# Kernel optimization log

Hardware: AMD Instinct MI355X
Metric: run time of the kernel (lower is better)

The kernel has to match this reference:

```python
import jax, jax.numpy as jnp
import numpy as np

N_NODES = 20000
N_EDGES = 640000
IN_NODE = 128
IN_EDGE = 16
HIDDEN = 64
OUT = 128
HEADS = 4
N_GRAPHS = 64
NEG_SLOPE = 0.2


def _glorot(key, shape):
    fan_in, fan_out = shape[0], shape[-1]
    s = jnp.sqrt(6.0 / (fan_in + fan_out)).astype(jnp.float32)
    return jax.random.uniform(key, shape, jnp.float32, -s, s)


def setup_inputs() -> dict:
    key = jax.random.key(0)
    ks = jax.random.split(key, 32)
    inp = {
        "x": jax.random.normal(ks[0], (N_NODES, IN_NODE), jnp.float32),
        "edge_attr": jax.random.normal(ks[1], (N_EDGES, IN_EDGE), jnp.float32),
        "edge_index": jax.random.randint(ks[2], (2, N_EDGES), 0, N_NODES),
        "batch": jnp.sort(jax.random.randint(ks[3], (N_NODES,), 0, N_GRAPHS)),
    }
    # layer dims: (in, out_per_head, concat)
    dims = [(IN_NODE, HIDDEN, True), (HIDDEN * HEADS, HIDDEN, True), (HIDDEN * HEADS, OUT, False)]
    k = 4
    for i, (cin, cout, concat) in enumerate(dims):
        hc = HEADS * cout
        inp[f"Wl{i}"] = _glorot(ks[k], (cin, hc)); k += 1
        inp[f"bl{i}"] = jnp.zeros((hc,), jnp.float32)
        inp[f"Wr{i}"] = _glorot(ks[k], (cin, hc)); k += 1
        inp[f"br{i}"] = jnp.zeros((hc,), jnp.float32)
        inp[f"We{i}"] = _glorot(ks[k], (IN_EDGE, hc)); k += 1
        inp[f"att{i}"] = _glorot(ks[k], (HEADS, cout)); k += 1
        inp[f"bias{i}"] = jnp.zeros((hc if concat else cout,), jnp.float32)
    return inp


def _gatv2_layer(x, edge_index, edge_attr, Wl, bl, Wr, br, We, att, bias, concat):
    """One PyG-style GATv2Conv layer with edge features."""
    H, C = att.shape
    N = x.shape[0]
    src, dst = edge_index[0], edge_index[1]
    xl = (x @ Wl + bl).reshape(N, H, C)  # messages from source
    xr = (x @ Wr + br).reshape(N, H, C)  # target query
    e = (edge_attr @ We).reshape(-1, H, C)
    m = jax.nn.leaky_relu(xl[src] + xr[dst] + e, NEG_SLOPE)  # [E,H,C]
    logits = jnp.einsum("ehc,hc->eh", m, att)  # [E,H]
    # scatter-softmax over edges grouped by destination node
    lmax = jax.ops.segment_max(logits, dst, num_segments=N)
    p = jnp.exp(logits - lmax[dst])
    denom = jax.ops.segment_sum(p, dst, num_segments=N)
    alpha = p / (denom[dst] + 1e-16)  # [E,H]
    out = jax.ops.segment_sum(alpha[:, :, None] * xl[src], dst, num_segments=N)  # [N,H,C]
    if concat:
        return out.reshape(N, H * C) + bias
    return out.mean(axis=1) + bias


def reference(x, edge_attr, edge_index, batch,
              Wl0, bl0, Wr0, br0, We0, att0, bias0,
              Wl1, bl1, Wr1, br1, We1, att1, bias1,
              Wl2, bl2, Wr2, br2, We2, att2, bias2):
    layers = [
        (Wl0, bl0, Wr0, br0, We0, att0, bias0, True),
        (Wl1, bl1, Wr1, br1, We1, att1, bias1, True),
        (Wl2, bl2, Wr2, br2, We2, att2, bias2, False),
    ]
    h = x
    for (Wl, bl, Wr, br, We, att, b, concat) in layers:
        h = _gatv2_layer(h, edge_index, edge_attr, Wl, bl, Wr, br, We, att, b, concat)
    # global max + mean pooling per graph
    x_max = jax.ops.segment_max(h, batch, num_segments=N_GRAPHS)
    s = jax.ops.segment_sum(h, batch, num_segments=N_GRAPHS)
    cnt = jax.ops.segment_sum(jnp.ones((h.shape[0], 1), h.dtype), batch, num_segments=N_GRAPHS)
    x_mean = s / jnp.maximum(cnt, 1.0)
    return jnp.concatenate([x_max, x_mean], axis=1)  # [G, 2*OUT]
```

## Files before the change

### kernel.cpp

```cpp
#include <hip/hip_runtime.h>

#define NB 8

typedef float f32x2 __attribute__((ext_vector_type(2)));

template <int K, int M>
__global__ __launch_bounds__(256) void node_gemm(
    const float* __restrict__ X, const float* __restrict__ W,
    const float* __restrict__ bias, float* __restrict__ Y) {
  constexpr int NPB = 16;
  constexpr int COLS4 = M / 4;
  constexpr int NG = 256 / COLS4;
  constexpr int RPN = NPB / NG;
  __shared__ float xs[NPB * K];
  const int tid = threadIdx.x;
  const int n0 = blockIdx.x * NPB;
  {
    const float4* X4 = reinterpret_cast<const float4*>(X + (size_t)n0 * K);
    float4* xs4 = reinterpret_cast<float4*>(xs);
    for (int i = tid; i < NPB * K / 4; i += 256) xs4[i] = X4[i];
  }
  __syncthreads();
  const int c4 = (tid % COLS4) * 4;
  const int r0 = (tid / COLS4) * RPN;
  float acc[RPN][4];
#pragma unroll
  for (int r = 0; r < RPN; ++r)
#pragma unroll
    for (int q = 0; q < 4; ++q) acc[r][q] = 0.f;

  for (int k = 0; k < K; k += 4) {
    float xv[RPN][4];
#pragma unroll
    for (int r = 0; r < RPN; ++r)
      *reinterpret_cast<float4*>(xv[r]) =
          *reinterpret_cast<const float4*>(&xs[(r0 + r) * K + k]);
#pragma unroll
    for (int j = 0; j < 4; ++j) {
      float wv[4];
      *reinterpret_cast<float4*>(wv) =
          *reinterpret_cast<const float4*>(&W[(size_t)(k + j) * M + c4]);
#pragma unroll
      for (int r = 0; r < RPN; ++r)
#pragma unroll
        for (int q = 0; q < 4; ++q)
          acc[r][q] = fmaf(xv[r][j], wv[q], acc[r][q]);
    }
  }
  float bv[4];
  *reinterpret_cast<float4*>(bv) = *reinterpret_cast<const float4*>(&bias[c4]);
#pragma unroll
  for (int r = 0; r < RPN; ++r) {
    float o[4];
#pragma unroll
    for (int q = 0; q < 4; ++q) o[q] = acc[r][q] + bv[q];
    *reinterpret_cast<float4*>(&Y[(size_t)(n0 + r0 + r) * M + c4]) =
        *reinterpret_cast<float4*>(o);
  }
}

__global__ void hist_b(const int* __restrict__ ei, int* __restrict__ kcnt,
                       int E, int bdiv) {
  int i = blockIdx.x * blockDim.x + threadIdx.x;
  if (i < E) atomicAdd(&kcnt[ei[E + i] * NB + ei[i] / bdiv], 1);
}

__global__ __launch_bounds__(1024) void blk_scan(
    const int* __restrict__ in, int* __restrict__ out1, int* __restrict__ bsum, int n) {
  __shared__ int buf[1024];
  const int tid = threadIdx.x;
  const int gid = blockIdx.x * 1024 + tid;
  int v = (gid < n) ? in[gid] : 0;
  buf[tid] = v;
  __syncthreads();
  for (int off = 1; off < 1024; off <<= 1) {
    int t = (tid >= off) ? buf[tid - off] : 0;
    __syncthreads();
    buf[tid] += t;
    __syncthreads();
  }
  if (gid < n) out1[gid] = buf[tid];
  if (tid == 1023) bsum[blockIdx.x] = buf[1023];
}

__global__ __launch_bounds__(256) void scan_bsum(int* __restrict__ bsum, int nb) {
  __shared__ int buf[256];
  const int tid = threadIdx.x;
  int v = (tid < nb) ? bsum[tid] : 0;
  buf[tid] = v;
  __syncthreads();
  for (int off = 1; off < 256; off <<= 1) {
    int t = (tid >= off) ? buf[tid - off] : 0;
    __syncthreads();
    buf[tid] += t;
    __syncthreads();
  }
  if (tid < nb) bsum[tid] = buf[tid];
}

__global__ void add_off(int* __restrict__ kptr, const int* __restrict__ bsum, int n) {
  int gid = blockIdx.x * blockDim.x + threadIdx.x;
  if (gid == 0) kptr[0] = 0;
  if (gid < n) {
    int blk = gid >> 10;
    if (blk > 0) kptr[1 + gid] += bsum[blk - 1];
  }
}

__global__ void csr_fill_b(const int* __restrict__ ei, const int* __restrict__ kptr,
                           int* __restrict__ kfill, int* __restrict__ csr_src,
                           int* __restrict__ csr_eid, int E, int bdiv) {
  int i = blockIdx.x * blockDim.x + threadIdx.x;
  if (i < E) {
    int src = ei[i], dst = ei[E + i];
    int key = dst * NB + src / bdiv;
    int slot = kptr[key] + atomicAdd(&kfill[key], 1);
    csr_src[slot] = src;
    csr_eid[slot] = i;
  }
}

__global__ void ea_perm(const float* __restrict__ ea, const int* __restrict__ csr_eid,
                        float* __restrict__ ea_csr, int E) {
  int i = blockIdx.x * blockDim.x + threadIdx.x;
  if (i < E * 16) {
    int slot = i >> 4;
    ea_csr[i] = ea[((size_t)csr_eid[slot] << 4) + (i & 15)];
  }
}

__global__ void graph_bounds(const int* __restrict__ batch, int* __restrict__ gstart,
                             int* __restrict__ gend, int N) {
  int i = blockIdx.x * blockDim.x + threadIdx.x;
  if (i < N) {
    int g = batch[i];
    atomicMin(&gstart[g], i);
    atomicMax(&gend[g], i + 1);
  }
}

template <int GS>
__device__ __forceinline__ void gat_edge_pk(
    const float4 a, const double (&c)[8], const float4 xrv,
    const f32x2 (&w01)[16], const f32x2 (&w23)[16], const float (&attv)[4],
    float& m, float& s, float (&acc)[4]) {
  f32x2 m01, m23;
  m01.x = a.x + xrv.x; m01.y = a.y + xrv.y;
  m23.x = a.z + xrv.z; m23.y = a.w + xrv.w;
#pragma unroll
  for (int i = 0; i < 8; ++i) {
    asm("v_pk_fma_f32 %0, %2, %3, %0 op_sel:[0,0,0] op_sel_hi:[0,1,1]\n\t"
        "v_pk_fma_f32 %1, %2, %4, %1 op_sel:[0,0,0] op_sel_hi:[0,1,1]\n\t"
        "v_pk_fma_f32 %0, %2, %5, %0 op_sel:[1,0,0] op_sel_hi:[1,1,1]\n\t"
        "v_pk_fma_f32 %1, %2, %6, %1 op_sel:[1,0,0] op_sel_hi:[1,1,1]"
        : "+v"(m01), "+v"(m23)
        : "s"(c[i]), "v"(w01[2 * i]), "v"(w23[2 * i]),
          "v"(w01[2 * i + 1]), "v"(w23[2 * i + 1]));
  }
  const float mv[4] = {m01.x, m01.y, m23.x, m23.y};
  float l = 0.f;
#pragma unroll
  for (int q = 0; q < 4; ++q) {
    const float v = fmaxf(mv[q], 0.2f * mv[q]);
    l = fmaf(v, attv[q], l);
  }
#pragma unroll
  for (int off = 1; off < GS; off <<= 1) l += __shfl_xor(l, off);
  const float nm = fmaxf(m, l);
  const float sc = __expf(m - nm);
  const float pe = __expf(l - nm);
  m = nm;
  s = fmaf(s, sc, pe);
  acc[0] = fmaf(pe, a.x, acc[0] * sc);
  acc[1] = fmaf(pe, a.y, acc[1] * sc);
  acc[2] = fmaf(pe, a.z, acc[2] * sc);
  acc[3] = fmaf(pe, a.w, acc[3] * sc);
}

template <int HCROW, int MODE>
__global__ __launch_bounds__(256) void fused_gat(
    const float* __restrict__ xl, const float* __restrict__ xr,
    const float* __restrict__ ea_csr, const float* __restrict__ We,
    const float* __restrict__ att, const float* __restrict__ bias,
    const int* __restrict__ kptr, const int* __restrict__ csr_src,
    float* __restrict__ out, float* __restrict__ outB, int N) {
  constexpr int C = HCROW / 4;
  constexpr int GS = C / 4;
  const int lane = threadIdx.x & 63;
  const int wslot = threadIdx.x >> 6;
  int bx = blockIdx.x;
  int colbase = 0;
  float* o_ptr = out;
  if (MODE == 1) {
    const int gb = gridDim.x >> 1;
    if (bx >= gb) { bx -= gb; colbase = 256; o_ptr = outB; }
  }
  const int dst = bx * 4 + wslot;
  if (dst >= N) return;

  f32x2 w01[16], w23[16];
#pragma unroll
  for (int k = 0; k < 16; ++k) {
    const float4 t =
        *reinterpret_cast<const float4*>(&We[k * HCROW + colbase + lane * 4]);
    w01[k].x = t.x; w01[k].y = t.y;
    w23[k].x = t.z; w23[k].y = t.w;
  }
  const int col0 = colbase + lane * 4;
  const int head = col0 / C;
  float attv[4];
  *reinterpret_cast<float4*>(attv) =
      *reinterpret_cast<const float4*>(&att[head * C + (col0 % C)]);
  const float4* xl4 = reinterpret_cast<const float4*>(xl);
  const int rs4 = HCROW / 4;
  const int coff = col0 >> 2;
  const float4 xrv =
      reinterpret_cast<const float4*>(xr)[(size_t)dst * rs4 + coff];
  const double* ed = reinterpret_cast<const double*>(ea_csr);

  const int row0 = __builtin_amdgcn_readfirstlane(kptr[dst * NB]);
  const int rend = __builtin_amdgcn_readfirstlane(kptr[dst * NB + NB]);

  float m = -__builtin_inff(), s = 0.f;
  float acc[4] = {0.f, 0.f, 0.f, 0.f};

  if (row0 < rend) {
    const int last = rend - 1;
    const int s0 = csr_src[row0];
    const int s1 = csr_src[min(row0 + 1, last)];
    const int s2 = csr_src[min(row0 + 2, last)];
    const int s3 = csr_src[min(row0 + 3, last)];
    float4 a0 = xl4[(size_t)s0 * rs4 + coff];
    float4 a1 = xl4[(size_t)s1 * rs4 + coff];
    float4 a2 = xl4[(size_t)s2 * rs4 + coff];
    float4 a3 = xl4[(size_t)s3 * rs4 + coff];
    int sr0 = csr_src[min(row0 + 4, last)];
    int sr1 = csr_src[min(row0 + 5, last)];
    double c0[8], c1[8];
    {
      const double* e0 = ed + (size_t)row0 * 8;
      const double* e1 = ed + (size_t)min(row0 + 1, last) * 8;
#pragma unroll
      for (int k = 0; k < 8; ++k) { c0[k] = e0[k]; c1[k] = e1[k]; }
    }

    for (int p = row0; p < rend; p += 2) {
      const float4 na0 = xl4[(size_t)sr0 * rs4 + coff];
      const float4 na1 = xl4[(size_t)sr1 * rs4 + coff];
      const int nsr0 = csr_src[min(p + 6, last)];
      const int nsr1 = csr_src[min(p + 7, last)];
      double cn0[8], cn1[8];
      {
        const double* e0 = ed + (size_t)min(p + 2, last) * 8;
        const double* e1 = ed + (size_t)min(p + 3, last) * 8;
#pragma unroll
        for (int k = 0; k < 8; ++k) { cn0[k] = e0[k]; cn1[k] = e1[k]; }
      }
      gat_edge_pk<GS>(a0, c0, xrv, w01, w23, attv, m, s, acc);
      if (p + 1 < rend) gat_edge_pk<GS>(a1, c1, xrv, w01, w23, attv, m, s, acc);
      a0 = a2; a1 = a3; a2 = na0; a3 = na1;
      sr0 = nsr0; sr1 = nsr1;
#pragma unroll
      for (int k = 0; k < 8; ++k) { c0[k] = cn0[k]; c1[k] = cn1[k]; }
    }
  }

  const float inv = 1.f / (s + 1e-16f);
  float o[4];
  if (MODE == 0) {
    float bv[4];
    *reinterpret_cast<float4*>(bv) = *reinterpret_cast<const float4*>(&bias[col0]);
#pragma unroll
    for (int q = 0; q < 4; ++q) o[q] = fmaf(acc[q], inv, bv[q]);
    *reinterpret_cast<float4*>(&o_ptr[(size_t)dst * HCROW + col0]) =
        *reinterpret_cast<float4*>(o);
  } else {
#pragma unroll
    for (int q = 0; q < 4; ++q) {
      o[q] = acc[q] * inv;
      o[q] += __shfl_xor(o[q], 32);
    }
    if (lane < 32)
      *reinterpret_cast<float4*>(&o_ptr[(size_t)dst * 128 + lane * 4]) =
          *reinterpret_cast<float4*>(o);
  }
}

__global__ __launch_bounds__(256) void pool_graph(
    const float* __restrict__ hA, const float* __restrict__ hB,
    const float* __restrict__ bias2, const int* __restrict__ gstart,
    const int* __restrict__ gend, float* __restrict__ out) {
  const int g = blockIdx.x;
  const int c = threadIdx.x & 127;
  const int sub = threadIdx.x >> 7;
  const int s0 = gstart[g], e0 = gend[g];
  const float b = bias2[c];
  float mx = -__builtin_inff(), sm = 0.f;
  for (int n = s0 + sub; n < e0; n += 2) {
    const float v = fmaf(0.25f, hA[(size_t)n * 128 + c] + hB[(size_t)n * 128 + c], b);
    mx = fmaxf(mx, v);
    sm += v;
  }
  __shared__ float smx[128], ssm[128];
  if (sub) { smx[c] = mx; ssm[c] = sm; }
  __syncthreads();
  if (!sub) {
    mx = fmaxf(mx, smx[c]);
    sm += ssm[c];
    const int cnt = e0 - s0;
    out[g * 256 + c] = (cnt > 0) ? mx : 0.f;
    out[g * 256 + 128 + c] = sm / fmaxf((float)cnt, 1.f);
  }
}

extern "C" void kernel_launch(void* const* d_in, const int* in_sizes, int n_in,
                              void* d_out, int out_size, void* d_ws, size_t ws_size,
                              hipStream_t stream) {
  const float* x     = (const float*)d_in[0];
  const float* ea    = (const float*)d_in[1];
  const int*   ei    = (const int*)d_in[2];
  const int*   batch = (const int*)d_in[3];
  const int N = in_sizes[0] / 128;
  const int E = in_sizes[2] / 2;
  const int NBINS = N * NB;
  const int bdiv = (N + NB - 1) / NB;

  const float* Wl[3]   = {(const float*)d_in[4],  (const float*)d_in[11], (const float*)d_in[18]};
  const float* blv[3]  = {(const float*)d_in[5],  (const float*)d_in[12], (const float*)d_in[19]};
  const float* Wr[3]   = {(const float*)d_in[6],  (const float*)d_in[13], (const float*)d_in[20]};
  const float* brv[3]  = {(const float*)d_in[7],  (const float*)d_in[14], (const float*)d_in[21]};
  const float* Wev[3]  = {(const float*)d_in[8],  (const float*)d_in[15], (const float*)d_in[22]};
  const float* attv[3] = {(const float*)d_in[9],  (const float*)d_in[16], (const float*)d_in[23]};
  const float* bias[3] = {(const float*)d_in[10], (const float*)d_in[17], (const float*)d_in[24]};

  float* ws = (float*)d_ws;
  float* xl     = ws;
  float* xr     = xl + (size_t)N * 512;
  float* ea_csr = xr + (size_t)N * 512;
  float* h      = ea_csr + (size_t)E * 16;
  int* kptr     = (int*)(h + (size_t)N * 256);
  int* csr_src  = kptr + (NBINS + 1);
  int* bsum     = csr_src + E;
  int* gstart   = bsum + 257;
  int* gend     = gstart + 64;
  int* csr_eid = (int*)h;
  int* kcnt    = csr_eid + E;
  int* kfill   = kcnt + NBINS;
  float* hsumA = h;
  float* hsumB = h + (size_t)N * 128;
  (void)n_in; (void)out_size; (void)ws_size;

  const int nodeBlocks = N / 16;
  const int edgeBlocks = (E + 255) / 256;
  const int scanBlocks = (NBINS + 1023) / 1024;
  const int gatBlocks = (N + 3) / 4;

  hipMemsetAsync(kcnt, 0, (size_t)2 * NBINS * sizeof(int), stream);
  hipMemsetAsync(gstart, 0x7f, 64 * sizeof(int), stream);
  hipMemsetAsync(gend, 0, 64 * sizeof(int), stream);
  hist_b<<<edgeBlocks, 256, 0, stream>>>(ei, kcnt, E, bdiv);
  graph_bounds<<<(N + 255) / 256, 256, 0, stream>>>(batch, gstart, gend, N);
  blk_scan<<<scanBlocks, 1024, 0, stream>>>(kcnt, kptr + 1, bsum, NBINS);
  scan_bsum<<<1, 256, 0, stream>>>(bsum, scanBlocks);
  add_off<<<(NBINS + 255) / 256, 256, 0, stream>>>(kptr, bsum, NBINS);
  csr_fill_b<<<edgeBlocks, 256, 0, stream>>>(ei, kptr, kfill, csr_src, csr_eid, E, bdiv);
  ea_perm<<<(E * 16 + 255) / 256, 256, 0, stream>>>(ea, csr_eid, ea_csr, E);

  node_gemm<128, 256><<<nodeBlocks, 256, 0, stream>>>(x, Wl[0], blv[0], xl);
  node_gemm<128, 256><<<nodeBlocks, 256, 0, stream>>>(x, Wr[0], brv[0], xr);
  fused_gat<256, 0><<<gatBlocks, 256, 0, stream>>>(
      xl, xr, ea_csr, Wev[0], attv[0], bias[0], kptr, csr_src, h, nullptr, N);

  node_gemm<256, 256><<<nodeBlocks, 256, 0, stream>>>(h, Wl[1], blv[1], xl);
  node_gemm<256, 256><<<nodeBlocks, 256, 0, stream>>>(h, Wr[1], brv[1], xr);
  fused_gat<256, 0><<<gatBlocks, 256, 0, stream>>>(
      xl, xr, ea_csr, Wev[1], attv[1], bias[1], kptr, csr_src, h, nullptr, N);

  node_gemm<256, 512><<<nodeBlocks, 256, 0, stream>>>(h, Wl[2], blv[2], xl);
  node_gemm<256, 512><<<nodeBlocks, 256, 0, stream>>>(h, Wr[2], brv[2], xr);
  fused_gat<512, 1><<<2 * gatBlocks, 256, 0, stream>>>(
      xl, xr, ea_csr, Wev[2], attv[2], bias[2], kptr, csr_src, hsumA, hsumB, N);

  pool_graph<<<64, 256, 0, stream>>>(hsumA, hsumB, bias[2], gstart, gend, (float*)d_out);
}
```

Baseline: 1.112 ms.

## Stage edge attributes in LDS chunks with double buffering in fused GAT

Edge attributes are no longer read by every lane as uniform scalar double loads. Each wave now cooperatively loads chunks of 32 edges' attributes into shared memory, prefetching the next chunk into registers while the current one is processed. The packed FMA takes its edge coefficient from a VGPR instead of an SGPR, and mode-1 blocks are interleaved so both column halves of a node run on adjacent blocks. NB is doubled (finer key binning) and the block-sum scan is widened to match. The cost is LDS traffic and VGPR pressure in exchange for fewer scalar memory loads.

```diff
diff --git a/kernel.cpp b/kernel.cpp
--- a/kernel.cpp
+++ b/kernel.cpp
@@ -1,6 +1,7 @@
 #include <hip/hip_runtime.h>
 
-#define NB 8
+#define NB 16
+#define CHUNK 32
 
 typedef float f32x2 __attribute__((ext_vector_type(2)));
 
@@ -83,13 +84,13 @@
   if (tid == 1023) bsum[blockIdx.x] = buf[1023];
 }
 
-__global__ __launch_bounds__(256) void scan_bsum(int* __restrict__ bsum, int nb) {
-  __shared__ int buf[256];
+__global__ __launch_bounds__(1024) void scan_bsum(int* __restrict__ bsum, int nb) {
+  __shared__ int buf[1024];
   const int tid = threadIdx.x;
   int v = (tid < nb) ? bsum[tid] : 0;
   buf[tid] = v;
   __syncthreads();
-  for (int off = 1; off < 256; off <<= 1) {
+  for (int off = 1; off < 1024; off <<= 1) {
     int t = (tid >= off) ? buf[tid - off] : 0;
     __syncthreads();
     buf[tid] += t;
@@ -141,7 +142,7 @@
 
 template <int GS>
 __device__ __forceinline__ void gat_edge_pk(
-    const float4 a, const double (&c)[8], const float4 xrv,
+    const float4 a, const f32x2 (&c)[8], const float4 xrv,
     const f32x2 (&w01)[16], const f32x2 (&w23)[16], const float (&attv)[4],
     float& m, float& s, float (&acc)[4]) {
   f32x2 m01, m23;
@@ -154,7 +155,7 @@
         "v_pk_fma_f32 %0, %2, %5, %0 op_sel:[1,0,0] op_sel_hi:[1,1,1]\n\t"
         "v_pk_fma_f32 %1, %2, %6, %1 op_sel:[1,0,0] op_sel_hi:[1,1,1]"
         : "+v"(m01), "+v"(m23)
-        : "s"(c[i]), "v"(w01[2 * i]), "v"(w23[2 * i]),
+        : "v"(c[i]), "v"(w01[2 * i]), "v"(w23[2 * i]),
           "v"(w01[2 * i + 1]), "v"(w23[2 * i + 1]));
   }
   const float mv[4] = {m01.x, m01.y, m23.x, m23.y};
@@ -186,14 +187,16 @@
     float* __restrict__ out, float* __restrict__ outB, int N) {
   constexpr int C = HCROW / 4;
   constexpr int GS = C / 4;
+  __shared__ float ea_s[4][2][CHUNK * 16];
   const int lane = threadIdx.x & 63;
   const int wslot = threadIdx.x >> 6;
   int bx = blockIdx.x;
   int colbase = 0;
   float* o_ptr = out;
   if (MODE == 1) {
-    const int gb = gridDim.x >> 1;
-    if (bx >= gb) { bx -= gb; colbase = 256; o_ptr = outB; }
+    colbase = (bx & 1) * 256;
+    if (bx & 1) o_ptr = outB;
+    bx >>= 1;
   }
   const int dst = bx * 4 + wslot;
   if (dst >= N) return;
@@ -216,7 +219,6 @@
   const int coff = col0 >> 2;
   const float4 xrv =
       reinterpret_cast<const float4*>(xr)[(size_t)dst * rs4 + coff];
-  const double* ed = reinterpret_cast<const double*>(ea_csr);
 
   const int row0 = __builtin_amdgcn_readfirstlane(kptr[dst * NB]);
   const int rend = __builtin_amdgcn_readfirstlane(kptr[dst * NB + NB]);
@@ -226,42 +228,57 @@
 
   if (row0 < rend) {
     const int last = rend - 1;
-    const int s0 = csr_src[row0];
-    const int s1 = csr_src[min(row0 + 1, last)];
-    const int s2 = csr_src[min(row0 + 2, last)];
-    const int s3 = csr_src[min(row0 + 3, last)];
-    float4 a0 = xl4[(size_t)s0 * rs4 + coff];
-    float4 a1 = xl4[(size_t)s1 * rs4 + coff];
-    float4 a2 = xl4[(size_t)s2 * rs4 + coff];
-    float4 a3 = xl4[(size_t)s3 * rs4 + coff];
-    int sr0 = csr_src[min(row0 + 4, last)];
-    int sr1 = csr_src[min(row0 + 5, last)];
-    double c0[8], c1[8];
     {
-      const double* e0 = ed + (size_t)row0 * 8;
-      const double* e1 = ed + (size_t)min(row0 + 1, last) * 8;
-#pragma unroll
-      for (int k = 0; k < 8; ++k) { c0[k] = e0[k]; c1[k] = e1[k]; }
+      const int n4 = min(CHUNK, rend - row0) * 4;
+      const float4* esrc = reinterpret_cast<const float4*>(ea_csr + (size_t)row0 * 16);
+      float4* ed = reinterpret_cast<float4*>(ea_s[wslot][0]);
+      if (lane < n4) ed[lane] = esrc[lane];
+      if (lane + 64 < n4) ed[lane + 64] = esrc[lane + 64];
     }
-
-    for (int p = row0; p < rend; p += 2) {
-      const float4 na0 = xl4[(size_t)sr0 * rs4 + coff];
-      const float4 na1 = xl4[(size_t)sr1 * rs4 + coff];
-      const int nsr0 = csr_src[min(p + 6, last)];
-      const int nsr1 = csr_src[min(p + 7, last)];
-      double cn0[8], cn1[8];
-      {
-        const double* e0 = ed + (size_t)min(p + 2, last) * 8;
-        const double* e1 = ed + (size_t)min(p + 3, last) * 8;
-#pragma unroll
-        for (int k = 0; k < 8; ++k) { cn0[k] = e0[k]; cn1[k] = e1[k]; }
+    int buf = 0;
+    for (int cs = row0; cs < rend; cs += CHUNK) {
+      const int cn = min(CHUNK, rend - cs);
+      float4 t0, t1;
+      int nn4 = 0;
+      if (cs + CHUNK < rend) {
+        nn4 = min(CHUNK, rend - (cs + CHUNK)) * 4;
+        const float4* esrc =
+            reinterpret_cast<const float4*>(ea_csr + (size_t)(cs + CHUNK) * 16);
+        if (lane < nn4) t0 = esrc[lane];
+        if (lane + 64 < nn4) t1 = esrc[lane + 64];
       }
-      gat_edge_pk<GS>(a0, c0, xrv, w01, w23, attv, m, s, acc);
-      if (p + 1 < rend) gat_edge_pk<GS>(a1, c1, xrv, w01, w23, attv, m, s, acc);
-      a0 = a2; a1 = a3; a2 = na0; a3 = na1;
-      sr0 = nsr0; sr1 = nsr1;
-#pragma unroll
-      for (int k = 0; k < 8; ++k) { c0[k] = cn0[k]; c1[k] = cn1[k]; }
+      const f32x2* eb = reinterpret_cast<const f32x2*>(ea_s[wslot][buf]);
+
+      int s0 = csr_src[cs];
+      int s1 = csr_src[min(cs + 1, last)];
+      float4 a0 = xl4[(size_t)s0 * rs4 + coff];
+      float4 a1 = xl4[(size_t)s1 * rs4 + coff];
+      int sr0 = csr_src[min(cs + 2, last)];
+      int sr1 = csr_src[min(cs + 3, last)];
+
+      for (int j = 0; j < cn; j += 2) {
+        const float4 na0 = xl4[(size_t)sr0 * rs4 + coff];
+        const float4 na1 = xl4[(size_t)sr1 * rs4 + coff];
+        const int nsr0 = csr_src[min(cs + j + 4, last)];
+        const int nsr1 = csr_src[min(cs + j + 5, last)];
+        f32x2 c0[8], c1[8];
+#pragma unroll
+        for (int i = 0; i < 8; ++i) {
+          c0[i] = eb[j * 8 + i];
+          c1[i] = eb[(j + 1) * 8 + i];
+        }
+        gat_edge_pk<GS>(a0, c0, xrv, w01, w23, attv, m, s, acc);
+        if (j + 1 < cn) gat_edge_pk<GS>(a1, c1, xrv, w01, w23, attv, m, s, acc);
+        a0 = na0; a1 = na1;
+        sr0 = nsr0; sr1 = nsr1;
+      }
+
+      if (nn4 > 0) {
+        float4* ed = reinterpret_cast<float4*>(ea_s[wslot][buf ^ 1]);
+        if (lane < nn4) ed[lane] = t0;
+        if (lane + 64 < nn4) ed[lane + 64] = t1;
+        buf ^= 1;
+      }
     }
   }
 
@@ -341,7 +358,7 @@
   int* kptr     = (int*)(h + (size_t)N * 256);
   int* csr_src  = kptr + (NBINS + 1);
   int* bsum     = csr_src + E;
-  int* gstart   = bsum + 257;
+  int* gstart   = bsum + 1024;
   int* gend     = gstart + 64;
   int* csr_eid = (int*)h;
   int* kcnt    = csr_eid + E;
@@ -361,7 +378,7 @@
   hist_b<<<edgeBlocks, 256, 0, stream>>>(ei, kcnt, E, bdiv);
   graph_bounds<<<(N + 255) / 256, 256, 0, stream>>>(batch, gstart, gend, N);
   blk_scan<<<scanBlocks, 1024, 0, stream>>>(kcnt, kptr + 1, bsum, NBINS);
-  scan_bsum<<<1, 256, 0, stream>>>(bsum, scanBlocks);
+  scan_bsum<<<1, 1024, 0, stream>>>(bsum, scanBlocks);
   add_off<<<(NBINS + 255) / 256, 256, 0, stream>>>(kptr, bsum, NBINS);
   csr_fill_b<<<edgeBlocks, 256, 0, stream>>>(ei, kptr, kfill, csr_src, csr_eid, E, bdiv);
   ea_perm<<<(E * 16 + 255) / 256, 256, 0, stream>>>(ea, csr_eid, ea_csr, E);
```

After: 1.152 ms. 3.6% more time.

## Split each destination's edge list across two waves with online-softmax merge

Applied to the files above, without the earlier changes.

Each destination node is now processed by two waves, each covering half of its CSR edge range, and their partial softmax states (max, sum, accumulators) are merged through shared memory. This doubles wave-level parallelism and halves per-wave serial edge latency in the fused GAT kernel. The CSR bin factor NB also goes from 8 to 16, and the bsum scan buffer and workspace offset are enlarged to match. The cost is an extra block sync, shared-memory traffic, and twice the per-wave setup, including the We register loads.

```diff
diff --git a/kernel.cpp b/kernel.cpp
--- a/kernel.cpp
+++ b/kernel.cpp
@@ -1,6 +1,6 @@
 #include <hip/hip_runtime.h>
 
-#define NB 8
+#define NB 16
 
 typedef float f32x2 __attribute__((ext_vector_type(2)));
 
@@ -83,13 +83,13 @@
   if (tid == 1023) bsum[blockIdx.x] = buf[1023];
 }
 
-__global__ __launch_bounds__(256) void scan_bsum(int* __restrict__ bsum, int nb) {
-  __shared__ int buf[256];
+__global__ __launch_bounds__(1024) void scan_bsum(int* __restrict__ bsum, int nb) {
+  __shared__ int buf[1024];
   const int tid = threadIdx.x;
   int v = (tid < nb) ? bsum[tid] : 0;
   buf[tid] = v;
   __syncthreads();
-  for (int off = 1; off < 256; off <<= 1) {
+  for (int off = 1; off < 1024; off <<= 1) {
     int t = (tid >= off) ? buf[tid - off] : 0;
     __syncthreads();
     buf[tid] += t;
@@ -186,17 +186,20 @@
     float* __restrict__ out, float* __restrict__ outB, int N) {
   constexpr int C = HCROW / 4;
   constexpr int GS = C / 4;
+  __shared__ float mrg[2][64][6];
   const int lane = threadIdx.x & 63;
   const int wslot = threadIdx.x >> 6;
+  const int dpair = wslot >> 1;
+  const int half = wslot & 1;
   int bx = blockIdx.x;
   int colbase = 0;
   float* o_ptr = out;
   if (MODE == 1) {
-    const int gb = gridDim.x >> 1;
-    if (bx >= gb) { bx -= gb; colbase = 256; o_ptr = outB; }
-  }
-  const int dst = bx * 4 + wslot;
-  if (dst >= N) return;
+    colbase = (bx & 1) * 256;
+    if (bx & 1) o_ptr = outB;
+    bx >>= 1;
+  }
+  const int dst = bx * 2 + dpair;
 
   f32x2 w01[16], w23[16];
 #pragma unroll
@@ -218,8 +221,11 @@
       reinterpret_cast<const float4*>(xr)[(size_t)dst * rs4 + coff];
   const double* ed = reinterpret_cast<const double*>(ea_csr);
 
-  const int row0 = __builtin_amdgcn_readfirstlane(kptr[dst * NB]);
-  const int rend = __builtin_amdgcn_readfirstlane(kptr[dst * NB + NB]);
+  const int r0f = __builtin_amdgcn_readfirstlane(kptr[dst * NB]);
+  const int rendf = __builtin_amdgcn_readfirstlane(kptr[dst * NB + NB]);
+  const int mid = r0f + ((rendf - r0f + 1) >> 1);
+  const int row0 = half ? mid : r0f;
+  const int rend = half ? rendf : mid;
 
   float m = -__builtin_inff(), s = 0.f;
   float acc[4] = {0.f, 0.f, 0.f, 0.f};
@@ -265,6 +271,28 @@
     }
   }
 
+  if (half) {
+    mrg[dpair][lane][0] = m;
+    mrg[dpair][lane][1] = s;
+    mrg[dpair][lane][2] = acc[0];
+    mrg[dpair][lane][3] = acc[1];
+    mrg[dpair][lane][4] = acc[2];
+    mrg[dpair][lane][5] = acc[3];
+  }
+  __syncthreads();
+  if (half) return;
+  {
+    const float m1 = mrg[dpair][lane][0];
+    const float s1 = mrg[dpair][lane][1];
+    const float nm = fmaxf(m, m1);
+    const float sc0 = (m > -1e37f) ? __expf(m - nm) : 0.f;
+    const float sc1 = (m1 > -1e37f) ? __expf(m1 - nm) : 0.f;
+    s = s * sc0 + s1 * sc1;
+#pragma unroll
+    for (int q = 0; q < 4; ++q)
+      acc[q] = acc[q] * sc0 + mrg[dpair][lane][2 + q] * sc1;
+  }
+
   const float inv = 1.f / (s + 1e-16f);
   float o[4];
   if (MODE == 0) {
@@ -341,7 +369,7 @@
   int* kptr     = (int*)(h + (size_t)N * 256);
   int* csr_src  = kptr + (NBINS + 1);
   int* bsum     = csr_src + E;
-  int* gstart   = bsum + 257;
+  int* gstart   = bsum + 1024;
   int* gend     = gstart + 64;
   int* csr_eid = (int*)h;
   int* kcnt    = csr_eid + E;
@@ -353,7 +381,7 @@
   const int nodeBlocks = N / 16;
   const int edgeBlocks = (E + 255) / 256;
   const int scanBlocks = (NBINS + 1023) / 1024;
-  const int gatBlocks = (N + 3) / 4;
+  const int gatBlocks = N / 2;
 
   hipMemsetAsync(kcnt, 0, (size_t)2 * NBINS * sizeof(int), stream);
   hipMemsetAsync(gstart, 0x7f, 64 * sizeof(int), stream);
@@ -361,7 +389,7 @@
   hist_b<<<edgeBlocks, 256, 0, stream>>>(ei, kcnt, E, bdiv);
   graph_bounds<<<(N + 255) / 256, 256, 0, stream>>>(batch, gstart, gend, N);
   blk_scan<<<scanBlocks, 1024, 0, stream>>>(kcnt, kptr + 1, bsum, NBINS);
-  scan_bsum<<<1, 256, 0, stream>>>(bsum, scanBlocks);
+  scan_bsum<<<1, 1024, 0, stream>>>(bsum, scanBlocks);
   add_off<<<(NBINS + 255) / 256, 256, 0, stream>>>(kptr, bsum, NBINS);
   csr_fill_b<<<edgeBlocks, 256, 0, stream>>>(ei, kptr, kfill, csr_src, csr_eid, E, bdiv);
   ea_perm<<<(E * 16 + 255) / 256, 256, 0, stream>>>(ea, csr_eid, ea_csr, E);
```

Result: slower. 1.450 ms (+30.4%).
